# Kernel tuning notes

Hardware: AMD Instinct MI355X
Metric: run time of the kernel (lower is better)

Reference implementation:

```python
import jax, jax.numpy as jnp
import numpy as np

B, T, N, D = 4, 24, 2048, 128
H = 4
HD = D // H
E = 8
K = 2
INTER = 512            # dim * mlp_ratio
MINTER = INTER // K    # per-expert intermediate (512//2 = 256)
EPS = 1e-6
ALPHA = 0.05           # GCN residual mixing
SCALE = HD ** -0.5


def setup_inputs() -> dict:
    key = jax.random.key(0)
    ks = jax.random.split(key, 32)
    w = lambda i, shape: (jax.random.normal(ks[i], shape, jnp.float32) * 0.02)
    inp = {
        "x": jax.random.normal(ks[0], (B, T, N, D), jnp.float32),
        "k": jax.random.normal(ks[1], (B, T, N, D), jnp.float32),
        "v": jax.random.normal(ks[2], (B, T, N, D), jnp.float32),
        "adj": jax.random.uniform(ks[3], (N, N), jnp.float32),
        # attention qkv projections (torch Linear: y = x @ W.T + b)
        "Wq": w(4, (D, D)), "bq": jnp.zeros((D,), jnp.float32),
        "Wk": w(5, (D, D)), "bk": jnp.zeros((D,), jnp.float32),
        "Wv": w(6, (D, D)), "bv": jnp.zeros((D,), jnp.float32),
        "norm_tatt_w": jnp.ones((D,), jnp.float32),
        # GCN
        "gcn_fc1_w": w(7, (D, D)),
        "gcn_mlp_w": w(8, (D, D)), "gcn_mlp_b": jnp.zeros((D,), jnp.float32),
        # block norms
        "norm1_w": jnp.ones((D,), jnp.float32),
        "norm2_w": jnp.ones((D,), jnp.float32),
        # MoE
        "gate_w": w(9, (E, D)),
        "ew1": w(10, (E, MINTER, D)),
        "ew2": w(11, (E, D, MINTER)),
        "ew3": w(12, (E, MINTER, D)),
        "sw1": w(13, (INTER, D)),
        "sw2": w(14, (D, INTER)),
        "sw3": w(15, (INTER, D)),
        "sgate_w": w(16, (1, D)),
    }
    return inp


def rms_norm(x, w):
    var = jnp.mean(x * x, axis=-1, keepdims=True)
    return w * (x * jax.lax.rsqrt(var + EPS))


def swiglu(x, w1, w2, w3):
    return (jax.nn.silu(x @ w1.T) * (x @ w3.T)) @ w2.T


def reference(x, k, v, adj, Wq, bq, Wk, bk, Wv, bv, norm_tatt_w,
              gcn_fc1_w, gcn_mlp_w, gcn_mlp_b, norm1_w, norm2_w,
              gate_w, ew1, ew2, ew3, sw1, sw2, sw3, sgate_w):
    # ---- pre-norm ----
    x_n = rms_norm(x, norm1_w)
    k_n = rms_norm(k, norm1_w)

    # ---- temporal self-attention (per node, over T) ----
    def heads(y, W, b):  # [B,T,N,D] -> [B,N,H,T,hd]
        y = y @ W.T + b
        return y.transpose(0, 2, 1, 3).reshape(B, N, -1, H, HD).transpose(0, 1, 3, 2, 4)

    q = heads(x_n, Wq, bq)
    kk = heads(k_n, Wk, bk)
    vv = heads(k_n, Wv, bv)  # module passes k for both k and v
    attn = jnp.einsum('bnhqd,bnhkd->bnhqk', q, kk) * SCALE
    attn = jax.nn.softmax(attn, axis=-1)
    t_x = jnp.einsum('bnhqk,bnhkd->bnhqd', attn, vv)
    t_x = t_x.transpose(0, 3, 1, 2, 4).reshape(B, T, N, D)  # [B,T,N,D]
    t_x = rms_norm(t_x, norm_tatt_w)

    # ---- GCN: row-normalized adjacency over node axis ----
    a = adj / jnp.sum(adj, axis=1, keepdims=True)            # a[n,k] = adj[n,k]/d[n]
    mixed = jnp.einsum('nk,btkd->btnd', a, t_x)
    gcn_out = mixed @ gcn_fc1_w.T
    out = ALPHA * t_x + (1.0 - ALPHA) * gcn_out
    ho = out @ gcn_mlp_w.T + gcn_mlp_b

    x = x + ho  # residual (drop_path = identity)

    # ---- MoE sparse experts ----
    x2 = rms_norm(x, norm2_w).reshape(-1, D)                 # [Tok, D]
    router_logits = x2 @ gate_w.T                            # [Tok, E]
    rw = jax.nn.softmax(router_logits.astype(jnp.float32), axis=-1)
    top_w, top_idx = jax.lax.top_k(rw, K)                    # [Tok, K]
    top_w = top_w.astype(x2.dtype)

    final = jnp.zeros_like(x2)
    for e in range(E):  # fixed small expert count
        coef = jnp.sum(jnp.where(top_idx == e, top_w, 0.0), axis=-1)  # [Tok]
        final = final + coef[:, None] * swiglu(x2, ew1[e], ew2[e], ew3[e])

    shared = swiglu(x2, sw1, sw2, sw3)
    shared = jax.nn.sigmoid(x2 @ sgate_w.T) * shared
    final = final + shared

    x = x + final.reshape(B, T, N, D)
    return x, router_logits
```

## Files before the change

kernel.cpp:

```cpp
#include <hip/hip_runtime.h>

#define BB 4
#define TT 24
#define NN 2048
#define DD 128
#define HH 4
#define HD 32
#define TOK 196608
#define EE 8
#define MINTER 256
#define INTER 512

typedef unsigned short u16;
typedef __attribute__((ext_vector_type(8))) short  bf16x8;
typedef __attribute__((ext_vector_type(4))) float  f32x4;
typedef __attribute__((ext_vector_type(4))) unsigned int u32x4;

#define MFMA(a,b,c) __builtin_amdgcn_mfma_f32_16x16x32_bf16((a),(b),(c),0,0,0)
#define AS(n) __attribute__((address_space(n)))

static __device__ __forceinline__ u16 f2b(float f) {
    union { float f; unsigned u; } v; v.f = f;
    unsigned r = v.u + 0x7FFFu + ((v.u >> 16) & 1u);
    return (u16)(r >> 16);
}
static __device__ __forceinline__ u16 f2b_fast(float f) {
    union { float f; unsigned u; } v; v.f = f;
    return (u16)(v.u >> 16);
}
static __device__ __forceinline__ float b2f(u16 b) {
    union { unsigned u; float f; } v; v.u = ((unsigned)b) << 16;
    return v.f;
}
static __device__ __forceinline__ float silu_mul(float u, float v) {
    return u * __builtin_amdgcn_rcpf(1.f + __expf(-u)) * v;
}

template<int C>
static __device__ __forceinline__ bf16x8 frag_ld(const u16* s, int row, int kbyte) {
    constexpr int mask = ((C/8) < 8 ? (C/8) : 8) - 1;
    int byte = row * (C * 2) + (kbyte ^ ((row & mask) << 4));
    return *(const bf16x8*)((const char*)s + byte);
}
template<int C>
static __device__ __forceinline__ u16 lds_us(const u16* s, int r, int c) {
    constexpr int mask = ((C/8) < 8 ? (C/8) : 8) - 1;
    int byte = r * (C * 2) + ((((c >> 3) << 4) ^ ((r & mask) << 4))) + ((c & 7) << 1);
    return *(const u16*)((const char*)s + byte);
}
template<int C>
static __device__ __forceinline__ void lds_store_us(u16* s, int r, int c, u16 v) {
    constexpr int mask = ((C/8) < 8 ? (C/8) : 8) - 1;
    int byte = r * (C * 2) + ((((c >> 3) << 4) ^ ((r & mask) << 4))) + ((c & 7) << 1);
    *(u16*)((char*)s + byte) = v;
}
static __device__ __forceinline__ bf16x8 frag_ld_p80(const u16* s, int row, int kbyte) {
    return *(const bf16x8*)((const char*)s + row * 80 + kbyte);
}
static __device__ __forceinline__ void sh_store_p80(u16* s, int r, int c, u16 v) {
    *(u16*)((char*)s + r * 80 + c * 2) = v;
}
template<int C>
static __device__ __forceinline__ void stage_bf16(u16* s, const u16* g, int gstride,
                                                  int rows, int tid, int nthr) {
    constexpr int cpr = C / 8;
    constexpr int mask = (cpr < 8 ? cpr : 8) - 1;
    for (int i = tid; i < rows * cpr; i += nthr) {
        int r = i / cpr, cc = i - r * cpr;
        u32x4 v = *(const u32x4*)(g + (size_t)r * gstride + cc * 8);
        *(u32x4*)((char*)s + r * (C * 2) + ((cc * 16) ^ ((r & mask) << 4))) = v;
    }
}
static __device__ __forceinline__ void stage_rms(u16* sA, const float* __restrict__ in,
        const float* __restrict__ nw, int tid) {
    int wid = tid >> 6, lane = tid & 63;
    float2 wv = *(const float2*)(nw + lane * 2);
    for (int rr = 0; rr < 32; ++rr) {
        int r = wid * 32 + rr;
        float2 v = *(const float2*)(in + (size_t)r * 128 + lane * 2);
        float ss = v.x * v.x + v.y * v.y;
        #pragma unroll
        for (int o = 32; o > 0; o >>= 1) ss += __shfl_xor(ss, o);
        float sc = rsqrtf(ss * (1.f / 128.f) + 1e-6f);
        unsigned pack = ((unsigned)f2b(v.y * sc * wv.y) << 16) | (unsigned)f2b(v.x * sc * wv.x);
        int byte = r * 256 + (((lane >> 2) * 16) ^ ((r & 7) << 4)) + ((lane & 3) << 2);
        *(unsigned*)((char*)sA + byte) = pack;
    }
}
static __device__ __forceinline__ void stage_async64(u16* s, const u16* g, int wi, int lane) {
    int slot = wi * 64 + lane;
    int r = slot >> 3, c = slot & 7;
    const u16* src = g + r * 2048 + ((c ^ (r & 7)) << 3);
    __builtin_amdgcn_global_load_lds((const AS(1) void*)src,
                                     (AS(3) void*)(s + wi * 512), 16, 0, 0);
}
static __device__ __forceinline__ void stage_img(u16* buf, const u16* img, int wid, int lane) {
    #pragma unroll
    for (int t = 0; t < 7; ++t) {
        int wi = wid + t * 4;
        if (wi < 26)
            __builtin_amdgcn_global_load_lds((const AS(1) void*)(img + wi * 512 + lane * 8),
                                             (AS(3) void*)(buf + wi * 512), 16, 0, 0);
    }
}
static __device__ __forceinline__ void zero_acc(f32x4 acc[4][4]) {
    f32x4 z = {0.f, 0.f, 0.f, 0.f};
    #pragma unroll
    for (int i = 0; i < 4; ++i)
        #pragma unroll
        for (int j = 0; j < 4; ++j) acc[i][j] = z;
}
template<int CA, int CB>
static __device__ __forceinline__ void gemm_step64(const u16* sA, const u16* sB,
        int arow0, int brow0, int kbyte, f32x4 acc[4][4], int ln15) {
    bf16x8 a[4], b[4];
    #pragma unroll
    for (int i = 0; i < 4; ++i) a[i] = frag_ld<CA>(sA, arow0 + i * 16 + ln15, kbyte);
    #pragma unroll
    for (int j = 0; j < 4; ++j) b[j] = frag_ld<CB>(sB, brow0 + j * 16 + ln15, kbyte);
    #pragma unroll
    for (int i = 0; i < 4; ++i)
        #pragma unroll
        for (int j = 0; j < 4; ++j)
            acc[i][j] = MFMA(a[i], b[j], acc[i][j]);
}

static __device__ __forceinline__ void swiglu_chunk(const u16* buf, u16* sH,
        const bf16x8 av[2][4], f32x4 aout[2][8],
        int wid, int g16, int ln15) {
    const u16* W1c = buf;
    const u16* W3c = buf + 4096;
    const u16* W2c = buf + 8192;
    f32x4 z = {0.f, 0.f, 0.f, 0.f};
    f32x4 a1[2][2], a3[2][2];
    #pragma unroll
    for (int mf = 0; mf < 2; ++mf)
        #pragma unroll
        for (int nf = 0; nf < 2; ++nf) { a1[mf][nf] = z; a3[mf][nf] = z; }
    __builtin_amdgcn_s_setprio(1);
    #pragma unroll
    for (int ks = 0; ks < 4; ++ks) {
        int kb = ks * 64 + g16 * 16;
        #pragma unroll
        for (int nf = 0; nf < 2; ++nf) {
            bf16x8 b1 = frag_ld<128>(W1c, nf * 16 + ln15, kb);
            bf16x8 b3 = frag_ld<128>(W3c, nf * 16 + ln15, kb);
            a1[0][nf] = MFMA(av[0][ks], b1, a1[0][nf]);
            a1[1][nf] = MFMA(av[1][ks], b1, a1[1][nf]);
            a3[0][nf] = MFMA(av[0][ks], b3, a3[0][nf]);
            a3[1][nf] = MFMA(av[1][ks], b3, a3[1][nf]);
        }
    }
    __builtin_amdgcn_s_setprio(0);
    #pragma unroll
    for (int mf = 0; mf < 2; ++mf)
        #pragma unroll
        for (int nf = 0; nf < 2; ++nf)
            #pragma unroll
            for (int r = 0; r < 4; ++r) {
                int row = wid * 32 + mf * 16 + g16 * 4 + r;
                int col = nf * 16 + ln15;
                sh_store_p80(sH, row, col, f2b_fast(silu_mul(a1[mf][nf][r], a3[mf][nf][r])));
            }
    asm volatile("s_waitcnt lgkmcnt(0)" ::: "memory");
    __builtin_amdgcn_sched_barrier(0);
    {
        int kb = g16 * 16;
        bf16x8 ah0 = frag_ld_p80(sH, wid * 32 + ln15, kb);
        bf16x8 ah1 = frag_ld_p80(sH, wid * 32 + 16 + ln15, kb);
        __builtin_amdgcn_s_setprio(1);
        #pragma unroll
        for (int nf = 0; nf < 8; ++nf) {
            bf16x8 bw = frag_ld_p80(W2c, nf * 16 + ln15, kb);
            aout[0][nf] = MFMA(ah0, bw, aout[0][nf]);
            aout[1][nf] = MFMA(ah1, bw, aout[1][nf]);
        }
        __builtin_amdgcn_s_setprio(0);
    }
}

__global__ __launch_bounds__(256) void preconvert(
        const float* __restrict__ Wq, const float* __restrict__ Wk,
        const float* __restrict__ Wv, const float* __restrict__ g1,
        const float* __restrict__ g2,
        const float* __restrict__ e1, const float* __restrict__ e2,
        const float* __restrict__ e3,
        const float* __restrict__ s1, const float* __restrict__ s2,
        const float* __restrict__ s3,
        u16* __restrict__ arena, int* __restrict__ cnts) {
    int idx = blockIdx.x * 256 + threadIdx.x;
    if (blockIdx.x == 0 && threadIdx.x < 8) cnts[threadIdx.x] = 0;
    if (idx < 20480) {
        int s = idx >> 12, rel = idx & 4095;
        const float* src = (s == 0) ? Wq : (s == 1) ? Wk : (s == 2) ? Wv : (s == 3) ? g1 : g2;
        const float4 v = *(const float4*)(src + (size_t)rel * 4);
        union { unsigned long long q; u16 us[4]; } o;
        o.us[0] = f2b(v.x); o.us[1] = f2b(v.y); o.us[2] = f2b(v.z); o.us[3] = f2b(v.w);
        *(unsigned long long*)(arena + (size_t)idx * 4) = o.q;
        return;
    }
    int p = idx - 20480;
    if (p >= 133120) return;
    const float *w1s, *w3s, *w2s_; int w2stride, ic;
    u16* img;
    if (p < 106496) {
        int imgIdx = p / 1664;
        p -= imgIdx * 1664;
        int e = imgIdx >> 3; ic = imgIdx & 7;
        w1s = e1 + (size_t)e * 32768;
        w3s = e3 + (size_t)e * 32768;
        w2s_ = e2 + (size_t)e * 32768;
        w2stride = 256;
        img = arena + 81920 + (size_t)imgIdx * 13312;
    } else {
        int q = p - 106496;
        int imgIdx = q / 1664; ic = imgIdx;
        p = q - imgIdx * 1664;
        w1s = s1; w3s = s3; w2s_ = s2; w2stride = 512;
        img = arena + 933888 + (size_t)imgIdx * 13312;
    }
    const float* src;
    if (p < 1024) {
        const float* wsrc = (p < 512) ? w1s : w3s;
        int pp = p & 511;
        int r = pp >> 4, chq = pp & 15;
        int cc = chq ^ (r & 7);
        src = wsrc + (size_t)(ic * 32 + r) * 128 + cc * 8;
    } else {
        int q = p - 1024;
        int r = q / 5, cc = q - r * 5;
        if (cc == 4) {
            u32x4 zv = {0, 0, 0, 0};
            *(u32x4*)(img + (size_t)p * 8) = zv;
            return;
        }
        src = w2s_ + (size_t)r * w2stride + ic * 32 + cc * 8;
    }
    union { u32x4 v; u16 us[8]; } o;
    #pragma unroll
    for (int j = 0; j < 8; ++j) o.us[j] = f2b(src[j]);
    *(u32x4*)(img + (size_t)p * 8) = o.v;
}

__global__ __launch_bounds__(256) void proj_rms(
        const float* __restrict__ xin, const u16* __restrict__ W,
        const float* __restrict__ bias, const float* __restrict__ nw,
        u16* __restrict__ out) {
    int tok0 = blockIdx.x * 128;
    __shared__ u16 sA[128 * 128];
    __shared__ u16 sW[128 * 128];
    int tid = threadIdx.x, lane = tid & 63, ln15 = lane & 15, g16 = lane >> 4, wid = tid >> 6;
    int wm = (wid >> 1) * 64, wn = (wid & 1) * 64;
    stage_rms(sA, xin + (size_t)tok0 * 128, nw, tid);
    stage_bf16<128>(sW, W, 128, 128, tid, 256);
    __syncthreads();
    f32x4 acc[4][4];
    zero_acc(acc);
    #pragma unroll
    for (int ks = 0; ks < 4; ++ks)
        gemm_step64<128, 128>(sA, sW, wm, wn, ks * 64 + g16 * 16, acc, ln15);
    #pragma unroll
    for (int j = 0; j < 4; ++j) {
        int col = wn + j * 16 + ln15;
        float bv = bias[col];
        #pragma unroll
        for (int i = 0; i < 4; ++i)
            #pragma unroll
            for (int r = 0; r < 4; ++r) {
                int row = wm + i * 16 + g16 * 4 + r;
                out[(size_t)(tok0 + row) * 128 + col] = f2b(acc[i][j][r] + bv);
            }
    }
}

__global__ __launch_bounds__(256) void projkv_rms(
        const float* __restrict__ kin, const u16* __restrict__ Wk,
        const float* __restrict__ bk, const u16* __restrict__ Wv,
        const float* __restrict__ bv, const float* __restrict__ nw,
        u16* __restrict__ kout, u16* __restrict__ vout) {
    int tok0 = blockIdx.x * 128;
    __shared__ u16 sA[128 * 128];
    __shared__ u16 sW[128 * 128];
    int tid = threadIdx.x, lane = tid & 63, ln15 = lane & 15, g16 = lane >> 4, wid = tid >> 6;
    int wm = (wid >> 1) * 64, wn = (wid & 1) * 64;
    stage_rms(sA, kin + (size_t)tok0 * 128, nw, tid);
    stage_bf16<128>(sW, Wk, 128, 128, tid, 256);
    __syncthreads();
    f32x4 acc[4][4];
    zero_acc(acc);
    #pragma unroll
    for (int ks = 0; ks < 4; ++ks)
        gemm_step64<128, 128>(sA, sW, wm, wn, ks * 64 + g16 * 16, acc, ln15);
    #pragma unroll
    for (int j = 0; j < 4; ++j) {
        int col = wn + j * 16 + ln15;
        float bvv = bk[col];
        #pragma unroll
        for (int i = 0; i < 4; ++i)
            #pragma unroll
            for (int r = 0; r < 4; ++r) {
                int row = wm + i * 16 + g16 * 4 + r;
                kout[(size_t)(tok0 + row) * 128 + col] = f2b(acc[i][j][r] + bvv);
            }
    }
    __syncthreads();
    stage_bf16<128>(sW, Wv, 128, 128, tid, 256);
    __syncthreads();
    zero_acc(acc);
    #pragma unroll
    for (int ks = 0; ks < 4; ++ks)
        gemm_step64<128, 128>(sA, sW, wm, wn, ks * 64 + g16 * 16, acc, ln15);
    #pragma unroll
    for (int j = 0; j < 4; ++j) {
        int col = wn + j * 16 + ln15;
        float bvv = bv[col];
        #pragma unroll
        for (int i = 0; i < 4; ++i)
            #pragma unroll
            for (int r = 0; r < 4; ++r) {
                int row = wm + i * 16 + g16 * 4 + r;
                vout[(size_t)(tok0 + row) * 128 + col] = f2b(acc[i][j][r] + bvv);
            }
    }
}

__global__ __launch_bounds__(256) void attn_kernel(
        const u16* __restrict__ q, const u16* __restrict__ kk, const u16* __restrict__ vv,
        const float* __restrict__ ntw, u16* __restrict__ txn) {
    int bid = blockIdx.x;
    int b = bid >> 11;
    int n = bid & 2047;
    __shared__ u16 sQ[4][24][32];
    __shared__ u16 sK[4][24][32];
    __shared__ u16 sV[4][24][32];
    __shared__ float sS[4][24][24];
    __shared__ float sO[24][128];
    int tid = threadIdx.x, lane = tid & 63, wid = tid >> 6;
    for (int idx = tid; idx < 3072; idx += 256) {
        int h = idx / 768;
        int rem = idx - h * 768;
        int t = rem >> 5;
        int d = rem & 31;
        size_t off = ((size_t)((b * 24 + t) * 2048 + n)) * 128 + h * 32 + d;
        sQ[h][t][d] = q[off];
        sK[h][t][d] = kk[off];
        sV[h][t][d] = vv[off];
    }
    __syncthreads();
    int h = wid;
    for (int i = lane; i < 576; i += 64) {
        int qi = i / 24, ki = i - qi * 24;
        float s = 0.f;
        #pragma unroll
        for (int c = 0; c < 32; ++c) s += b2f(sQ[h][qi][c]) * b2f(sK[h][ki][c]);
        sS[h][qi][ki] = s * 0.17677669529663687f;
    }
    __syncthreads();
    if (lane < 24) {
        float m = -1e30f;
        #pragma unroll
        for (int c = 0; c < 24; ++c) m = fmaxf(m, sS[h][lane][c]);
        float e[24]; float sum = 0.f;
        #pragma unroll
        for (int c = 0; c < 24; ++c) { e[c] = __expf(sS[h][lane][c] - m); sum += e[c]; }
        float inv = 1.f / sum;
        #pragma unroll
        for (int c = 0; c < 24; ++c) sS[h][lane][c] = e[c] * inv;
    }
    __syncthreads();
    for (int i = lane; i < 768; i += 64) {
        int qi = i >> 5, d = i & 31;
        float acc = 0.f;
        #pragma unroll
        for (int c = 0; c < 24; ++c) acc += sS[h][qi][c] * b2f(sV[h][c][d]);
        sO[qi][h * 32 + d] = acc;
    }
    __syncthreads();
    for (int j = 0; j < 6; ++j) {
        int t = wid * 6 + j;
        float v0 = sO[t][lane], v1 = sO[t][lane + 64];
        float ss = v0 * v0 + v1 * v1;
        #pragma unroll
        for (int o = 32; o > 0; o >>= 1) ss += __shfl_xor(ss, o);
        float sc = rsqrtf(ss * (1.f / 128.f) + 1e-6f);
        size_t off = ((size_t)((b * 24 + t) * 2048 + n)) * 128;
        txn[off + lane]      = f2b(v0 * sc * ntw[lane]);
        txn[off + lane + 64] = f2b(v1 * sc * ntw[lane + 64]);
    }
}

__global__ __launch_bounds__(256) void adj_norm(const float* __restrict__ adj, u16* __restrict__ abf) {
    int nrow = blockIdx.x;
    const float* r = adj + (size_t)nrow * 2048;
    int tid = threadIdx.x;
    float s = 0.f;
    for (int c = tid; c < 2048; c += 256) s += r[c];
    __shared__ float red[4];
    #pragma unroll
    for (int o = 32; o > 0; o >>= 1) s += __shfl_xor(s, o);
    if ((tid & 63) == 0) red[tid >> 6] = s;
    __syncthreads();
    float inv = 1.f / (red[0] + red[1] + red[2] + red[3]);
    u16* o = abf + (size_t)nrow * 2048;
    for (int c = tid; c < 2048; c += 256) o[c] = f2b(r[c] * inv);
}

__global__ __launch_bounds__(256) void transpose_k(const u16* __restrict__ txn, u16* __restrict__ txT) {
    int bt = blockIdx.x >> 5;
    int n0 = (blockIdx.x & 31) * 64;
    int tid = threadIdx.x;
    int nn = tid & 63, dg = tid >> 6;
    for (int rep = 0; rep < 4; ++rep) {
        int d0 = rep * 32 + dg * 8;
        union { u32x4 v; u16 us[8]; } u;
        u.v = *(const u32x4*)(txn + ((size_t)(bt * 2048 + n0 + nn)) * 128 + d0);
        #pragma unroll
        for (int j = 0; j < 8; ++j)
            txT[((size_t)(bt * 128 + d0 + j)) * 2048 + n0 + nn] = u.us[j];
    }
}

__global__ __launch_bounds__(256) void gcn_gemm(
        const u16* __restrict__ abf, const u16* __restrict__ txT, u16* __restrict__ mixed) {
    int bt = blockIdx.x >> 4;
    int n0 = (blockIdx.x & 15) * 128;
    __shared__ u16 sA[128 * 64];
    __shared__ u16 sB[128 * 64];
    int tid = threadIdx.x, lane = tid & 63, ln15 = lane & 15, g16 = lane >> 4, wid = tid >> 6;
    int wm = (wid >> 1) * 64, wn = (wid & 1) * 64;
    f32x4 acc[4][4];
    zero_acc(acc);
    const u16* aRow = abf + (size_t)n0 * 2048;
    const u16* bRow = txT + (size_t)bt * 128 * 2048;
    for (int k0 = 0; k0 < 2048; k0 += 64) {
        __syncthreads();
        #pragma unroll
        for (int i = 0; i < 4; ++i) stage_async64(sA, aRow + k0, wid * 4 + i, lane);
        #pragma unroll
        for (int i = 0; i < 4; ++i) stage_async64(sB, bRow + k0, wid * 4 + i, lane);
        __syncthreads();
        #pragma unroll
        for (int ks = 0; ks < 2; ++ks)
            gemm_step64<64, 64>(sA, sB, wm, wn, ks * 64 + g16 * 16, acc, ln15);
    }
    u16* out = mixed + ((size_t)(bt * 2048 + n0)) * 128;
    #pragma unroll
    for (int i = 0; i < 4; ++i)
        #pragma unroll
        for (int j = 0; j < 4; ++j)
            #pragma unroll
            for (int r = 0; r < 4; ++r) {
                int row = wm + i * 16 + g16 * 4 + r;
                int col = wn + j * 16 + ln15;
                out[(size_t)row * 128 + col] = f2b(acc[i][j][r]);
            }
}

__global__ __launch_bounds__(256) void fused_gcn_router(
        const u16* __restrict__ mixed, const u16* __restrict__ txn,
        const float* __restrict__ x,
        const u16* __restrict__ W1, const u16* __restrict__ W2,
        const float* __restrict__ bias2, const float* __restrict__ n2w,
        const float* __restrict__ gatew,
        float* __restrict__ outx, float* __restrict__ outlog,
        u16* __restrict__ x2n,
        int* __restrict__ lists, float* __restrict__ listw, int* __restrict__ cnts) {
    int tok0 = blockIdx.x * 128;
    __shared__ char LB[65536];
    __shared__ float sGate[1024];
    __shared__ float sN2[128];
    __shared__ float sBias[128];
    __shared__ float sLog[1024];
    __shared__ float sPart[256];
    __shared__ float sScale[128];
    __shared__ int sBCnt[8];
    __shared__ int sGBase[8];
    u16* sM = (u16*)LB;
    u16* sW = (u16*)(LB + 32768);
    float* sXn = (float*)LB;
    int tid = threadIdx.x, lane = tid & 63, ln15 = lane & 15, g16 = lane >> 4, wid = tid >> 6;
    int wm = (wid >> 1) * 64, wn = (wid & 1) * 64;
    stage_bf16<128>(sM, mixed + (size_t)tok0 * 128, 128, 128, tid, 256);
    stage_bf16<128>(sW, W1, 128, 128, tid, 256);
    for (int i = tid; i < 1024; i += 256) sGate[i] = gatew[i];
    if (tid < 128) { sN2[tid] = n2w[tid]; sBias[tid] = bias2[tid]; }
    if (tid < 8) sBCnt[tid] = 0;
    __syncthreads();
    f32x4 acc[4][4];
    zero_acc(acc);
    #pragma unroll
    for (int ks = 0; ks < 4; ++ks)
        gemm_step64<128, 128>(sM, sW, wm, wn, ks * 64 + g16 * 16, acc, ln15);
    __syncthreads();
    stage_bf16<128>(sM, txn + (size_t)tok0 * 128, 128, 128, tid, 256);
    stage_bf16<128>(sW, W2, 128, 128, tid, 256);
    __syncthreads();
    #pragma unroll
    for (int i = 0; i < 4; ++i)
        #pragma unroll
        for (int j = 0; j < 4; ++j)
            #pragma unroll
            for (int r = 0; r < 4; ++r) {
                int row = wm + i * 16 + g16 * 4 + r;
                int col = wn + j * 16 + ln15;
                float tv = b2f(lds_us<128>(sM, row, col));
                lds_store_us<128>(sM, row, col, f2b(0.05f * tv + 0.95f * acc[i][j][r]));
            }
    __syncthreads();
    zero_acc(acc);
    #pragma unroll
    for (int ks = 0; ks < 4; ++ks)
        gemm_step64<128, 128>(sM, sW, wm, wn, ks * 64 + g16 * 16, acc, ln15);
    #pragma unroll
    for (int i = 0; i < 4; ++i)
        #pragma unroll
        for (int j = 0; j < 4; ++j)
            #pragma unroll
            for (int r = 0; r < 4; ++r) {
                int row = wm + i * 16 + g16 * 4 + r;
                int col = wn + j * 16 + ln15;
                float xv = x[(size_t)(tok0 + row) * 128 + col] + acc[i][j][r] + sBias[col];
                outx[(size_t)(tok0 + row) * 128 + col] = xv;
                acc[i][j][r] = xv;
            }
    #pragma unroll
    for (int i = 0; i < 4; ++i)
        #pragma unroll
        for (int r = 0; r < 4; ++r) {
            float s = 0.f;
            #pragma unroll
            for (int j = 0; j < 4; ++j) s += acc[i][j][r] * acc[i][j][r];
            s += __shfl_xor(s, 1); s += __shfl_xor(s, 2);
            s += __shfl_xor(s, 4); s += __shfl_xor(s, 8);
            if (ln15 == 0) sPart[(wm + i * 16 + g16 * 4 + r) * 2 + (wid & 1)] = s;
        }
    __syncthreads();
    if (tid < 128)
        sScale[tid] = rsqrtf((sPart[tid * 2] + sPart[tid * 2 + 1]) * (1.f / 128.f) + 1e-6f);
    __syncthreads();
    #pragma unroll
    for (int i = 0; i < 4; ++i)
        #pragma unroll
        for (int j = 0; j < 4; ++j)
            #pragma unroll
            for (int r = 0; r < 4; ++r) {
                int row = wm + i * 16 + g16 * 4 + r;
                int col = wn + j * 16 + ln15;
                sXn[row * 128 + col] = acc[i][j][r] * sScale[row] * sN2[col];
            }
    __syncthreads();
    {
        int r = tid >> 1, e0 = (tid & 1) * 4;
        float a0 = 0, a1 = 0, a2 = 0, a3 = 0;
        for (int cc = 0; cc < 128; ++cc) {
            int c = (cc + r) & 127;
            float v = sXn[r * 128 + c];
            a0 += v * sGate[(e0 + 0) * 128 + c];
            a1 += v * sGate[(e0 + 1) * 128 + c];
            a2 += v * sGate[(e0 + 2) * 128 + c];
            a3 += v * sGate[(e0 + 3) * 128 + c];
        }
        int rb = r * 8 + e0;
        sLog[rb + 0] = a0; sLog[rb + 1] = a1; sLog[rb + 2] = a2; sLog[rb + 3] = a3;
        size_t ob = (size_t)(tok0 + r) * 8 + e0;
        outlog[ob + 0] = a0; outlog[ob + 1] = a1; outlog[ob + 2] = a2; outlog[ob + 3] = a3;
    }
    for (int cc = tid; cc < 2048; cc += 256) {
        int r = cc >> 4, c0 = (cc & 15) * 8;
        union { u32x4 v; u16 us[8]; } u;
        #pragma unroll
        for (int jj = 0; jj < 8; ++jj) u.us[jj] = f2b(sXn[r * 128 + c0 + jj]);
        *(u32x4*)(x2n + (size_t)(tok0 + r) * 128 + c0) = u.v;
    }
    __syncthreads();
    int e1 = 0, e2 = 0, le1 = 0, le2 = 0;
    float w1v = 0.f, w2v = 0.f;
    if (tid < 128) {
        int r = tid;
        float l[8];
        #pragma unroll
        for (int e = 0; e < 8; ++e) l[e] = sLog[r * 8 + e];
        float m = l[0];
        #pragma unroll
        for (int e = 1; e < 8; ++e) m = fmaxf(m, l[e]);
        float ex[8]; float s = 0.f;
        #pragma unroll
        for (int e = 0; e < 8; ++e) { ex[e] = __expf(l[e] - m); s += ex[e]; }
        float inv = 1.f / s;
        float b1v = ex[0]; e1 = 0;
        #pragma unroll
        for (int e = 1; e < 8; ++e) if (ex[e] > b1v) { b1v = ex[e]; e1 = e; }
        e2 = (e1 == 0) ? 1 : 0; float b2v = ex[e2];
        #pragma unroll
        for (int e = 0; e < 8; ++e) if (e != e1 && ex[e] > b2v) { b2v = ex[e]; e2 = e; }
        w1v = b1v * inv; w2v = b2v * inv;
        le1 = atomicAdd(&sBCnt[e1], 1);
        le2 = atomicAdd(&sBCnt[e2], 1);
    }
    __syncthreads();
    if (tid < 8) sGBase[tid] = atomicAdd(&cnts[tid], sBCnt[tid]);
    __syncthreads();
    if (tid < 128) {
        int tok = tok0 + tid;
        int p1 = sGBase[e1] + le1;
        lists[(size_t)e1 * TOK + p1] = tok * 2 + 0; listw[(size_t)e1 * TOK + p1] = w1v;
        int p2 = sGBase[e2] + le2;
        lists[(size_t)e2 * TOK + p2] = tok * 2 + 1; listw[(size_t)e2 * TOK + p2] = w2v;
    }
}

__global__ __launch_bounds__(256, 2) void moe_expert(
        const u16* __restrict__ x2n, const int* __restrict__ lists,
        const float* __restrict__ listw, const int* __restrict__ cnts,
        const u16* __restrict__ eimg, u16* __restrict__ slotOut) {
    int e = blockIdx.y;
    int base = blockIdx.x * 128;
    int cnt = cnts[e];
    if (base >= cnt) return;
    int valid = min(128, cnt - base);
    const int* lst = lists + (size_t)e * TOK + base;
    const float* lw = listw + (size_t)e * TOK + base;
    __shared__ u16 sBufA[13312];
    __shared__ u16 sBufB[13312];
    __shared__ u16 sH[5120];
    __shared__ float sCoef[128];
    __shared__ int sTok[128];
    int tid = threadIdx.x, lane = tid & 63, ln15 = lane & 15, g16 = lane >> 4, wid = tid >> 6;
    const u16* imgbase = eimg + (size_t)(e * 8) * 13312;
    stage_img(sBufA, imgbase, wid, lane);
    if (tid < 128) {
        int t = (tid < valid) ? lst[tid] : -1;
        sTok[tid] = t;
        sCoef[tid] = (tid < valid) ? lw[tid] : 0.f;
    }
    __syncthreads();
    bf16x8 av[2][4];
    {
        bf16x8 zz = {0, 0, 0, 0, 0, 0, 0, 0};
        int t0 = sTok[wid * 32 + ln15];
        int t1 = sTok[wid * 32 + 16 + ln15];
        const u16* r0 = x2n + (size_t)(t0 >> 1) * 128;
        const u16* r1 = x2n + (size_t)(t1 >> 1) * 128;
        #pragma unroll
        for (int ks = 0; ks < 4; ++ks) {
            av[0][ks] = (t0 >= 0) ? *(const bf16x8*)(r0 + ks * 32 + g16 * 8) : zz;
            av[1][ks] = (t1 >= 0) ? *(const bf16x8*)(r1 + ks * 32 + g16 * 8) : zz;
        }
    }
    f32x4 aout[2][8];
    f32x4 z = {0.f, 0.f, 0.f, 0.f};
    #pragma unroll
    for (int mf = 0; mf < 2; ++mf)
        #pragma unroll
        for (int nf = 0; nf < 8; ++nf) aout[mf][nf] = z;
    for (int ic = 0; ic < 8; ++ic) {
        u16* cur = (ic & 1) ? sBufB : sBufA;
        u16* alt = (ic & 1) ? sBufA : sBufB;
        if (ic + 1 < 8)
            stage_img(alt, imgbase + (size_t)(ic + 1) * 13312, wid, lane);
        swiglu_chunk(cur, sH, av, aout, wid, g16, ln15);
        __syncthreads();
    }
    #pragma unroll
    for (int mf = 0; mf < 2; ++mf)
        #pragma unroll
        for (int nf = 0; nf < 8; ++nf)
            #pragma unroll
            for (int r = 0; r < 4; ++r) {
                int row = wid * 32 + mf * 16 + g16 * 4 + r;
                if (row < valid) {
                    int col = nf * 16 + ln15;
                    slotOut[(size_t)sTok[row] * 128 + col] = f2b_fast(sCoef[row] * aout[mf][nf][r]);
                }
            }
}

__global__ __launch_bounds__(256, 2) void moe_shared(
        const u16* __restrict__ x2n, const u16* __restrict__ simg,
        const float* __restrict__ sgw, const u16* __restrict__ slotOut,
        float* __restrict__ outx) {
    int tok0 = blockIdx.x * 128;
    __shared__ u16 sBufA[13312];
    __shared__ u16 sBufB[13312];
    __shared__ u16 sH[5120];
    __shared__ float sGv[128];
    int tid = threadIdx.x, lane = tid & 63, ln15 = lane & 15, g16 = lane >> 4, wid = tid >> 6;
    stage_img(sBufA, simg, wid, lane);
    bf16x8 av[2][4];
    {
        const u16* r0 = x2n + (size_t)(tok0 + wid * 32 + ln15) * 128;
        const u16* r1 = x2n + (size_t)(tok0 + wid * 32 + 16 + ln15) * 128;
        #pragma unroll
        for (int ks = 0; ks < 4; ++ks) {
            av[0][ks] = *(const bf16x8*)(r0 + ks * 32 + g16 * 8);
            av[1][ks] = *(const bf16x8*)(r1 + ks * 32 + g16 * 8);
        }
    }
    if (tid < 128) {
        const u16* xr = x2n + (size_t)(tok0 + tid) * 128;
        float d = 0.f;
        #pragma unroll
        for (int c8 = 0; c8 < 16; ++c8) {
            bf16x8 v = *(const bf16x8*)(xr + c8 * 8);
            #pragma unroll
            for (int j = 0; j < 8; ++j) d += b2f((u16)v[j]) * sgw[c8 * 8 + j];
        }
        sGv[tid] = 1.f / (1.f + __expf(-d));
    }
    f32x4 aout[2][8];
    f32x4 z = {0.f, 0.f, 0.f, 0.f};
    #pragma unroll
    for (int mf = 0; mf < 2; ++mf)
        #pragma unroll
        for (int nf = 0; nf < 8; ++nf) aout[mf][nf] = z;
    __syncthreads();
    for (int ic = 0; ic < 16; ++ic) {
        u16* cur = (ic & 1) ? sBufB : sBufA;
        u16* alt = (ic & 1) ? sBufA : sBufB;
        if (ic + 1 < 16)
            stage_img(alt, simg + (size_t)(ic + 1) * 13312, wid, lane);
        swiglu_chunk(cur, sH, av, aout, wid, g16, ln15);
        __syncthreads();
    }
    #pragma unroll
    for (int mf = 0; mf < 2; ++mf)
        #pragma unroll
        for (int nf = 0; nf < 8; ++nf)
            #pragma unroll
            for (int r = 0; r < 4; ++r) {
                int row = wid * 32 + mf * 16 + g16 * 4 + r;
                int col = nf * 16 + ln15;
                size_t t = (size_t)(tok0 + row);
                float fc = b2f(slotOut[(t * 2 + 0) * 128 + col])
                         + b2f(slotOut[(t * 2 + 1) * 128 + col]);
                size_t idx = t * 128 + col;
                outx[idx] = outx[idx] + fc + sGv[row] * aout[mf][nf][r];
            }
}

#define SZTD  ((size_t)TOK * 128 * 2)
#define OFF_XN   ((size_t)0)
#define OFF_KN   (SZTD)
#define OFF_Q    (SZTD * 2)
#define OFF_KP   (SZTD * 3)
#define OFF_VP   (SZTD * 4)
#define OFF_ABF  (SZTD * 5)
#define OFF_LW   (OFF_ABF + 8388608)
#define OFF_LIST (OFF_LW + (size_t)8 * TOK * 4)
#define OFF_CNT  (OFF_LIST + (size_t)8 * TOK * 4)
#define OFF_ARENA (OFF_CNT + 128)

extern "C" void kernel_launch(void* const* d_in, const int* in_sizes, int n_in,
                              void* d_out, int out_size, void* d_ws, size_t ws_size,
                              hipStream_t stream) {
    (void)in_sizes; (void)n_in; (void)out_size; (void)ws_size;
    const float* x    = (const float*)d_in[0];
    const float* k    = (const float*)d_in[1];
    const float* adj  = (const float*)d_in[3];
    const float* Wq   = (const float*)d_in[4];
    const float* bq   = (const float*)d_in[5];
    const float* Wk   = (const float*)d_in[6];
    const float* bk   = (const float*)d_in[7];
    const float* Wv   = (const float*)d_in[8];
    const float* bv   = (const float*)d_in[9];
    const float* ntw  = (const float*)d_in[10];
    const float* gfc1 = (const float*)d_in[11];
    const float* gmlp = (const float*)d_in[12];
    const float* gmlpb= (const float*)d_in[13];
    const float* n1w  = (const float*)d_in[14];
    const float* n2w  = (const float*)d_in[15];
    const float* gatew= (const float*)d_in[16];
    const float* ew1  = (const float*)d_in[17];
    const float* ew2  = (const float*)d_in[18];
    const float* ew3  = (const float*)d_in[19];
    const float* sw1  = (const float*)d_in[20];
    const float* sw2  = (const float*)d_in[21];
    const float* sw3  = (const float*)d_in[22];
    const float* sgw  = (const float*)d_in[23];

    char* ws = (char*)d_ws;
    u16*  xn   = (u16*)(ws + OFF_XN);
    u16*  kn   = (u16*)(ws + OFF_KN);
    u16*  qb   = (u16*)(ws + OFF_Q);
    u16*  kpb  = (u16*)(ws + OFF_KP);
    u16*  vpb  = (u16*)(ws + OFF_VP);
    u16*  slotOut = (u16*)(ws + OFF_KP);
    u16*  abf  = (u16*)(ws + OFF_ABF);
    float* lw  = (float*)(ws + OFF_LW);
    int*  lst  = (int*)(ws + OFF_LIST);
    int*  cnts = (int*)(ws + OFF_CNT);
    u16*  arena = (u16*)(ws + OFF_ARENA);
    u16*  bWq = arena;
    u16*  bWk = arena + 16384;
    u16*  bWv = arena + 32768;
    u16*  bG1 = arena + 49152;
    u16*  bG2 = arena + 65536;
    u16*  eimg = arena + 81920;
    u16*  simg = arena + 933888;
    float* outx   = (float*)d_out;
    float* outlog = outx + (size_t)TOK * 128;

    preconvert<<<600, 256, 0, stream>>>(Wq, Wk, Wv, gfc1, gmlp, ew1, ew2, ew3,
                                        sw1, sw2, sw3, arena, cnts);
    proj_rms<<<1536, 256, 0, stream>>>(x, bWq, bq, n1w, qb);
    projkv_rms<<<1536, 256, 0, stream>>>(k, bWk, bk, bWv, bv, n1w, kpb, vpb);
    attn_kernel<<<8192, 256, 0, stream>>>(qb, kpb, vpb, ntw, xn );
    adj_norm<<<2048, 256, 0, stream>>>(adj, abf);
    transpose_k<<<3072, 256, 0, stream>>>(xn, qb );
    gcn_gemm<<<1536, 256, 0, stream>>>(abf, qb, kn );
    fused_gcn_router<<<1536, 256, 0, stream>>>(kn, xn, x, bG1, bG2, gmlpb, n2w, gatew,
                                               outx, outlog, qb , lst, lw, cnts);
    moe_expert<<<dim3(1536, 8), 256, 0, stream>>>(qb, lst, lw, cnts, eimg, slotOut);
    moe_shared<<<1536, 256, 0, stream>>>(qb, simg, sgw, slotOut, outx);
}
```

Measured before the change: 731.3 us.

## Load W2 fragments straight to registers and shrink LDS buffers in MoE kernels

```diff
diff --git a/kernel.cpp b/kernel.cpp
--- a/kernel.cpp
+++ b/kernel.cpp
@@ -94,13 +94,12 @@
     __builtin_amdgcn_global_load_lds((const AS(1) void*)src,
                                      (AS(3) void*)(s + wi * 512), 16, 0, 0);
 }
-static __device__ __forceinline__ void stage_img(u16* buf, const u16* img, int wid, int lane) {
-    #pragma unroll
-    for (int t = 0; t < 7; ++t) {
+static __device__ __forceinline__ void stage_img16(u16* buf, const u16* img, int wid, int lane) {
+    #pragma unroll
+    for (int t = 0; t < 4; ++t) {
         int wi = wid + t * 4;
-        if (wi < 26)
-            __builtin_amdgcn_global_load_lds((const AS(1) void*)(img + wi * 512 + lane * 8),
-                                             (AS(3) void*)(buf + wi * 512), 16, 0, 0);
+        __builtin_amdgcn_global_load_lds((const AS(1) void*)(img + wi * 512 + lane * 8),
+                                         (AS(3) void*)(buf + wi * 512), 16, 0, 0);
     }
 }
 static __device__ __forceinline__ void zero_acc(f32x4 acc[4][4]) {
@@ -126,11 +125,10 @@
 }
 
 static __device__ __forceinline__ void swiglu_chunk(const u16* buf, u16* sH,
-        const bf16x8 av[2][4], f32x4 aout[2][8],
+        const bf16x8 av[2][4], const bf16x8 w2r[8], f32x4 aout[2][8],
         int wid, int g16, int ln15) {
     const u16* W1c = buf;
     const u16* W3c = buf + 4096;
-    const u16* W2c = buf + 8192;
     f32x4 z = {0.f, 0.f, 0.f, 0.f};
     f32x4 a1[2][2], a3[2][2];
     #pragma unroll
@@ -171,9 +169,8 @@
         __builtin_amdgcn_s_setprio(1);
         #pragma unroll
         for (int nf = 0; nf < 8; ++nf) {
-            bf16x8 bw = frag_ld_p80(W2c, nf * 16 + ln15, kb);
-            aout[0][nf] = MFMA(ah0, bw, aout[0][nf]);
-            aout[1][nf] = MFMA(ah1, bw, aout[1][nf]);
+            aout[0][nf] = MFMA(ah0, w2r[nf], aout[0][nf]);
+            aout[1][nf] = MFMA(ah1, w2r[nf], aout[1][nf]);
         }
         __builtin_amdgcn_s_setprio(0);
     }
@@ -200,46 +197,40 @@
         return;
     }
     int p = idx - 20480;
-    if (p >= 133120) return;
+    if (p >= 122880) return;
+    int imgIdx = p / 1536;
+    int ppos = p - imgIdx * 1536;
     const float *w1s, *w3s, *w2s_; int w2stride, ic;
     u16* img;
-    if (p < 106496) {
-        int imgIdx = p / 1664;
-        p -= imgIdx * 1664;
+    if (imgIdx < 64) {
         int e = imgIdx >> 3; ic = imgIdx & 7;
         w1s = e1 + (size_t)e * 32768;
         w3s = e3 + (size_t)e * 32768;
         w2s_ = e2 + (size_t)e * 32768;
         w2stride = 256;
-        img = arena + 81920 + (size_t)imgIdx * 13312;
+        img = arena + 81920 + (size_t)imgIdx * 12288;
     } else {
-        int q = p - 106496;
-        int imgIdx = q / 1664; ic = imgIdx;
-        p = q - imgIdx * 1664;
+        ic = imgIdx - 64;
         w1s = s1; w3s = s3; w2s_ = s2; w2stride = 512;
-        img = arena + 933888 + (size_t)imgIdx * 13312;
+        img = arena + 868352 + (size_t)ic * 12288;
     }
     const float* src;
-    if (p < 1024) {
-        const float* wsrc = (p < 512) ? w1s : w3s;
-        int pp = p & 511;
+    if (ppos < 1024) {
+        const float* wsrc = (ppos < 512) ? w1s : w3s;
+        int pp = ppos & 511;
         int r = pp >> 4, chq = pp & 15;
         int cc = chq ^ (r & 7);
         src = wsrc + (size_t)(ic * 32 + r) * 128 + cc * 8;
     } else {
-        int q = p - 1024;
-        int r = q / 5, cc = q - r * 5;
-        if (cc == 4) {
-            u32x4 zv = {0, 0, 0, 0};
-            *(u32x4*)(img + (size_t)p * 8) = zv;
-            return;
-        }
-        src = w2s_ + (size_t)r * w2stride + ic * 32 + cc * 8;
+        int q = ppos - 1024;
+        int nf = q >> 6, ln = q & 63;
+        int l15 = ln & 15, g = ln >> 4;
+        src = w2s_ + (size_t)(nf * 16 + l15) * w2stride + ic * 32 + g * 8;
     }
     union { u32x4 v; u16 us[8]; } o;
     #pragma unroll
     for (int j = 0; j < 8; ++j) o.us[j] = f2b(src[j]);
-    *(u32x4*)(img + (size_t)p * 8) = o.v;
+    *(u32x4*)(img + (size_t)ppos * 8) = o.v;
 }
 
 __global__ __launch_bounds__(256) void proj_rms(
@@ -609,7 +600,7 @@
     }
 }
 
-__global__ __launch_bounds__(256, 2) void moe_expert(
+__global__ __launch_bounds__(256, 3) void moe_expert(
         const u16* __restrict__ x2n, const int* __restrict__ lists,
         const float* __restrict__ listw, const int* __restrict__ cnts,
         const u16* __restrict__ eimg, u16* __restrict__ slotOut) {
@@ -620,14 +611,14 @@
     int valid = min(128, cnt - base);
     const int* lst = lists + (size_t)e * TOK + base;
     const float* lw = listw + (size_t)e * TOK + base;
-    __shared__ u16 sBufA[13312];
-    __shared__ u16 sBufB[13312];
+    __shared__ u16 sBufA[8192];
+    __shared__ u16 sBufB[8192];
     __shared__ u16 sH[5120];
     __shared__ float sCoef[128];
     __shared__ int sTok[128];
     int tid = threadIdx.x, lane = tid & 63, ln15 = lane & 15, g16 = lane >> 4, wid = tid >> 6;
-    const u16* imgbase = eimg + (size_t)(e * 8) * 13312;
-    stage_img(sBufA, imgbase, wid, lane);
+    const u16* imgbase = eimg + (size_t)(e * 8) * 12288;
+    stage_img16(sBufA, imgbase, wid, lane);
     if (tid < 128) {
         int t = (tid < valid) ? lst[tid] : -1;
         sTok[tid] = t;
@@ -656,9 +647,14 @@
     for (int ic = 0; ic < 8; ++ic) {
         u16* cur = (ic & 1) ? sBufB : sBufA;
         u16* alt = (ic & 1) ? sBufA : sBufB;
+        bf16x8 w2r[8];
+        const u16* w2img = imgbase + (size_t)ic * 12288 + 8192;
+        #pragma unroll
+        for (int nf = 0; nf < 8; ++nf)
+            w2r[nf] = *(const bf16x8*)(w2img + nf * 512 + lane * 8);
         if (ic + 1 < 8)
-            stage_img(alt, imgbase + (size_t)(ic + 1) * 13312, wid, lane);
-        swiglu_chunk(cur, sH, av, aout, wid, g16, ln15);
+            stage_img16(alt, imgbase + (size_t)(ic + 1) * 12288, wid, lane);
+        swiglu_chunk(cur, sH, av, w2r, aout, wid, g16, ln15);
         __syncthreads();
     }
     #pragma unroll
@@ -675,17 +671,17 @@
             }
 }
 
-__global__ __launch_bounds__(256, 2) void moe_shared(
+__global__ __launch_bounds__(256, 3) void moe_shared(
         const u16* __restrict__ x2n, const u16* __restrict__ simg,
         const float* __restrict__ sgw, const u16* __restrict__ slotOut,
         float* __restrict__ outx) {
     int tok0 = blockIdx.x * 128;
-    __shared__ u16 sBufA[13312];
-    __shared__ u16 sBufB[13312];
+    __shared__ u16 sBufA[8192];
+    __shared__ u16 sBufB[8192];
     __shared__ u16 sH[5120];
     __shared__ float sGv[128];
     int tid = threadIdx.x, lane = tid & 63, ln15 = lane & 15, g16 = lane >> 4, wid = tid >> 6;
-    stage_img(sBufA, simg, wid, lane);
+    stage_img16(sBufA, simg, wid, lane);
     bf16x8 av[2][4];
     {
         const u16* r0 = x2n + (size_t)(tok0 + wid * 32 + ln15) * 128;
@@ -717,9 +713,14 @@
     for (int ic = 0; ic < 16; ++ic) {
         u16* cur = (ic & 1) ? sBufB : sBufA;
         u16* alt = (ic & 1) ? sBufA : sBufB;
+        bf16x8 w2r[8];
+        const u16* w2img = simg + (size_t)ic * 12288 + 8192;
+        #pragma unroll
+        for (int nf = 0; nf < 8; ++nf)
+            w2r[nf] = *(const bf16x8*)(w2img + nf * 512 + lane * 8);
         if (ic + 1 < 16)
-            stage_img(alt, simg + (size_t)(ic + 1) * 13312, wid, lane);
-        swiglu_chunk(cur, sH, av, aout, wid, g16, ln15);
+            stage_img16(alt, simg + (size_t)(ic + 1) * 12288, wid, lane);
+        swiglu_chunk(cur, sH, av, w2r, aout, wid, g16, ln15);
         __syncthreads();
     }
     #pragma unroll
@@ -796,11 +797,11 @@
     u16*  bG1 = arena + 49152;
     u16*  bG2 = arena + 65536;
     u16*  eimg = arena + 81920;
-    u16*  simg = arena + 933888;
+    u16*  simg = arena + 868352;
     float* outx   = (float*)d_out;
     float* outlog = outx + (size_t)TOK * 128;
 
-    preconvert<<<600, 256, 0, stream>>>(Wq, Wk, Wv, gfc1, gmlp, ew1, ew2, ew3,
+    preconvert<<<560, 256, 0, stream>>>(Wq, Wk, Wv, gfc1, gmlp, ew1, ew2, ew3,
                                         sw1, sw2, sw3, arena, cnts);
     proj_rms<<<1536, 256, 0, stream>>>(x, bWq, bq, n1w, qb);
     projkv_rms<<<1536, 256, 0, stream>>>(k, bWk, bk, bWv, bv, n1w, kpb, vpb);
```

Result: slower. 850.3 us (+16.3%).
